# Performance work log

Hardware: AMD Instinct MI355X
Metric: run time of the kernel (lower is better)

Reference implementation:

```python
import jax, jax.numpy as jnp
import numpy as np

N_NODES = 10000
N_EDGES = 80000
OBS_DIMS = 128
HIDDEN = 1024
ACT_DIMS = 8
N_GRAPHS = 64


def setup_inputs() -> dict:
    key = jax.random.key(0)
    ks = jax.random.split(key, 8)
    x = jax.random.normal(ks[0], (N_NODES, OBS_DIMS), dtype=jnp.float32)
    edge_index = jax.random.randint(ks[1], (2, N_EDGES), 0, N_NODES, dtype=jnp.int64)
    batch = jnp.sort(jax.random.randint(ks[2], (N_NODES,), 0, N_GRAPHS, dtype=jnp.int64))
    # Glorot-style init for weights, zero bias (as in PyG GCNConv / Linear defaults)
    W1 = jax.random.normal(ks[3], (OBS_DIMS, HIDDEN), dtype=jnp.float32) * (1.0 / np.sqrt(OBS_DIMS))
    b1 = jnp.zeros((HIDDEN,), dtype=jnp.float32)
    W2 = jax.random.normal(ks[4], (HIDDEN, HIDDEN), dtype=jnp.float32) * (1.0 / np.sqrt(HIDDEN))
    b2 = jnp.zeros((HIDDEN,), dtype=jnp.float32)
    Wl = jax.random.normal(ks[5], (HIDDEN, ACT_DIMS), dtype=jnp.float32) * (1.0 / np.sqrt(HIDDEN))
    bl = jnp.zeros((ACT_DIMS,), dtype=jnp.float32)
    return {"x": x, "edge_index": edge_index, "batch": batch,
            "W1": W1, "b1": b1, "W2": W2, "b2": b2, "Wl": Wl, "bl": bl}


def _gcn_conv(x, src, dst, dinv, W, b, n):
    """PyG GCNConv: D^-1/2 (A+I) D^-1/2 X W + b (self-loops already in src/dst)."""
    h = x @ W                                   # [N, out]
    norm = (dinv[src] * dinv[dst])[:, None]      # [E+N, 1]
    msg = h[src] * norm                          # gather + scale
    out = jax.ops.segment_sum(msg, dst, num_segments=n)
    return out + b


def reference(x, edge_index, batch, W1, b1, W2, b2, Wl, bl):
    n = x.shape[0]
    loops = jnp.arange(n, dtype=edge_index.dtype)
    src = jnp.concatenate([edge_index[0], loops])  # add self-loops
    dst = jnp.concatenate([edge_index[1], loops])
    # degree (with self-loops) from destination column, as PyG does
    deg = jax.ops.segment_sum(jnp.ones_like(dst, dtype=x.dtype), dst, num_segments=n)
    dinv = jax.lax.rsqrt(jnp.maximum(deg, 1.0))

    h = jax.nn.relu(_gcn_conv(x, src, dst, dinv, W1, b1, n))
    h = _gcn_conv(h, src, dst, dinv, W2, b2, n)
    h = jnp.tanh(h @ Wl + bl)                    # [N, act_dims]

    # global_mean_pool over batch segment ids
    sums = jax.ops.segment_sum(h, batch, num_segments=N_GRAPHS)
    counts = jax.ops.segment_sum(jnp.ones((n, 1), h.dtype), batch, num_segments=N_GRAPHS)
    return sums / jnp.maximum(counts, 1.0)       # [N_GRAPHS, act_dims]
```

## Files before the change

kernel.cpp:

```cpp
#include <hip/hip_runtime.h>
#include <hip/hip_bf16.h>

#define NNODES 10000
#define NEDGES 80000
#define OBS    128
#define HID    1024
#define ACTD   8
#define NGR    64

typedef __bf16 bf16x8 __attribute__((ext_vector_type(8)));
typedef float  f32x4  __attribute__((ext_vector_type(4)));
typedef ushort us8    __attribute__((ext_vector_type(8)));
typedef const __attribute__((address_space(1))) unsigned int gl_u32;
typedef __attribute__((address_space(3))) unsigned int lds_u32;

__device__ __forceinline__ ushort f2b(float f) {
    union { float f; unsigned int i; } v; v.f = f;
    unsigned int lsb = (v.i >> 16) & 1u;
    unsigned int r = v.i + 0x7fffu + lsb;
    return (ushort)(r >> 16);
}
__device__ __forceinline__ int cix(int v, int hi) {
    return v < 0 ? 0 : (v >= hi ? hi - 1 : v);
}

__global__ __launch_bounds__(256) void k_prep(const float* __restrict__ W1,
                                              const float* __restrict__ W2,
                                              const float* __restrict__ Wl,
                                              const float* __restrict__ b2,
                                              const float* __restrict__ bl,
                                              ushort* __restrict__ Wt1,
                                              ushort* __restrict__ M2bf,
                                              float* __restrict__ b2l,
                                              float* __restrict__ zacc,
                                              float* __restrict__ pool,
                                              float* __restrict__ cnt,
                                              int* __restrict__ degi) {
    int blk = blockIdx.x;
    if (blk >= 385) {
        int idx = (blk - 385) * 256 + threadIdx.x;
        if (idx < NNODES * ACTD) zacc[idx] = 0.0f;
        if (idx < NGR * ACTD) pool[idx] = 0.0f;
        if (idx < NGR) cnt[idx] = 0.0f;
        if (idx < NNODES) degi[idx] = 0;
        return;
    }
    if (blk < 128) {
        __shared__ float tile[32][33];
        int bx = (blk & 31) * 32, by = (blk >> 5) * 32;
        int tx = threadIdx.x & 31, ty = threadIdx.x >> 5;
        #pragma unroll
        for (int i = 0; i < 32; i += 8)
            tile[ty + i][tx] = W1[(size_t)(by + ty + i) * HID + bx + tx];
        __syncthreads();
        #pragma unroll
        for (int i = 0; i < 32; i += 8)
            Wt1[(size_t)(bx + ty + i) * OBS + by + tx] = f2b(tile[tx][ty + i]);
        return;
    }
    int wvid = ((blk - 128) * 256 + (int)threadIdx.x) >> 6;
    int lane = threadIdx.x & 63;
    if (wvid > HID) return;
    const float* row = (wvid == HID) ? b2 : (W2 + (size_t)wvid * HID);
    float acc[ACTD];
    #pragma unroll
    for (int j = 0; j < ACTD; ++j) acc[j] = 0.0f;
    for (int it = 0; it < HID / 64; ++it) {
        int k = it * 64 + lane;
        float w2v = row[k];
        float4 a = *(const float4*)(Wl + (size_t)k * ACTD);
        float4 b = *(const float4*)(Wl + (size_t)k * ACTD + 4);
        acc[0] += w2v * a.x; acc[1] += w2v * a.y; acc[2] += w2v * a.z; acc[3] += w2v * a.w;
        acc[4] += w2v * b.x; acc[5] += w2v * b.y; acc[6] += w2v * b.z; acc[7] += w2v * b.w;
    }
    #pragma unroll
    for (int off = 32; off > 0; off >>= 1)
        #pragma unroll
        for (int j = 0; j < ACTD; ++j)
            acc[j] += __shfl_down(acc[j], off);
    if (lane == 0) {
        if (wvid == HID) {
            #pragma unroll
            for (int j = 0; j < ACTD; ++j) b2l[j] = acc[j] + bl[j];
        } else {
            #pragma unroll
            for (int j = 0; j < ACTD; ++j) M2bf[wvid * ACTD + j] = f2b(acc[j]);
        }
    }
}

__global__ void k_count(const int* __restrict__ dst, int* degi,
                        const float* __restrict__ xw, int e) {
    int i = blockIdx.x * 256 + threadIdx.x;
    if (i < e) atomicAdd(&degi[cix(dst[i], NNODES)], 1);
    float wacc = 0.0f;
    int stride = gridDim.x * 256;
    for (int k = i; k < NNODES * OBS / 4; k += stride) {
        float4 v = *((const float4*)xw + k);
        wacc += v.x + v.y + v.z + v.w;
    }
    asm volatile("" :: "v"(wacc));
}

__global__ __launch_bounds__(1024) void k_scan(const int* __restrict__ degi,
                                               int* rowptr, int* cursor, float* dinv) {
    __shared__ int wsum[16];
    int t = threadIdx.x, lane = t & 63, w = t >> 6;
    int base = t * 10;
    int local[10];
    int s = 0;
    #pragma unroll
    for (int k = 0; k < 10; ++k) {
        int i = base + k;
        int v = 0;
        if (i < NNODES) {
            v = degi[i];
            dinv[i] = rsqrtf((float)(v + 1));
        }
        local[k] = s; s += v;
    }
    int sc = s;
    #pragma unroll
    for (int off = 1; off < 64; off <<= 1) {
        int u = __shfl_up(sc, off);
        if (lane >= off) sc += u;
    }
    if (lane == 63) wsum[w] = sc;
    __syncthreads();
    if (w == 0 && lane < 16) {
        int v = wsum[lane];
        #pragma unroll
        for (int off = 1; off < 16; off <<= 1) {
            int u = __shfl_up(v, off);
            if (lane >= off) v += u;
        }
        wsum[lane] = v;
    }
    __syncthreads();
    int excl = ((w == 0) ? 0 : wsum[w - 1]) + (sc - s);
    #pragma unroll
    for (int k = 0; k < 10; ++k) {
        int i = base + k;
        if (i < NNODES) { rowptr[i] = excl + local[k]; cursor[i] = excl + local[k]; }
    }
    if (t == 0) rowptr[NNODES] = wsum[15];
}

__global__ void k_fill(const int* __restrict__ src, const int* __restrict__ dst,
                       const float* __restrict__ dinv, int* cursor,
                       int* __restrict__ esrc, float* __restrict__ coefs, int e) {
    int i = blockIdx.x * 256 + threadIdx.x;
    if (i >= e) return;
    int s = cix(src[i], NNODES), d = cix(dst[i], NNODES);
    int pos = atomicAdd(&cursor[d], 1);
    esrc[pos] = s;
    coefs[pos] = dinv[s] * dinv[d];
}

__global__ void k_aggx(const float* __restrict__ x, const float* __restrict__ dinv,
                       const int* __restrict__ rowptr, const int* __restrict__ esrc,
                       const float* __restrict__ coefs, ushort* __restrict__ aggbf, int n) {
    int wv = (blockIdx.x * 256 + threadIdx.x) >> 6;
    int lane = threadIdx.x & 63;
    if (wv >= n) return;
    int q = lane >> 4, c = lane & 15;
    float4 v0 = make_float4(0.f, 0.f, 0.f, 0.f), v1 = v0;
    if (q == 0) {
        float d = dinv[wv], d2 = d * d;
        const float* xs = x + (size_t)wv * OBS + c * 8;
        float4 a0 = *(const float4*)(xs);
        float4 a1 = *(const float4*)(xs + 4);
        v0.x = a0.x * d2; v0.y = a0.y * d2; v0.z = a0.z * d2; v0.w = a0.w * d2;
        v1.x = a1.x * d2; v1.y = a1.y * d2; v1.z = a1.z * d2; v1.w = a1.w * d2;
    }
    int e1 = rowptr[wv + 1];
    for (int e = rowptr[wv] + q; e < e1; e += 4) {
        int s = esrc[e];
        float cf = coefs[e];
        const float* xs = x + (size_t)s * OBS + c * 8;
        float4 a0 = *(const float4*)(xs);
        float4 a1 = *(const float4*)(xs + 4);
        v0.x += a0.x * cf; v0.y += a0.y * cf; v0.z += a0.z * cf; v0.w += a0.w * cf;
        v1.x += a1.x * cf; v1.y += a1.y * cf; v1.z += a1.z * cf; v1.w += a1.w * cf;
    }
    #pragma unroll
    for (int off = 16; off <= 32; off <<= 1) {
        v0.x += __shfl_xor(v0.x, off); v0.y += __shfl_xor(v0.y, off);
        v0.z += __shfl_xor(v0.z, off); v0.w += __shfl_xor(v0.w, off);
        v1.x += __shfl_xor(v1.x, off); v1.y += __shfl_xor(v1.y, off);
        v1.z += __shfl_xor(v1.z, off); v1.w += __shfl_xor(v1.w, off);
    }
    if (q == 0) {
        us8 o;
        o[0] = f2b(v0.x); o[1] = f2b(v0.y); o[2] = f2b(v0.z); o[3] = f2b(v0.w);
        o[4] = f2b(v1.x); o[5] = f2b(v1.y); o[6] = f2b(v1.z); o[7] = f2b(v1.w);
        *(us8*)(aggbf + (size_t)wv * OBS + c * 8) = o;
    }
}

__global__ __launch_bounds__(256) void k_gemm1_fused(const ushort* __restrict__ A,
                                                     const ushort* __restrict__ Bt,
                                                     const float* __restrict__ bias,
                                                     const ushort* __restrict__ M2bf,
                                                     float* __restrict__ zacc,
                                                     int M) {
    __shared__ ushort buf[128 * 136 + 16 * 128];
    ushort* As    = buf;
    ushort* Bs    = buf + 8192;
    ushort* stage = buf;
    ushort* M2t   = buf + 128 * 136;

    const int t = threadIdx.x;
    const int bm = blockIdx.x, bn = blockIdx.y;
    const int lane = t & 63, wv = t >> 6;
    const int wm = (wv & 1) * 64, wn = (wv >> 1) * 64;
    const int l16 = lane & 15, kg = (lane >> 4) * 8;

    if (t < 128) {
        ushort4 a = *(const ushort4*)(M2bf + (size_t)(bn * 128 + t) * ACTD);
        ushort4 b = *(const ushort4*)(M2bf + (size_t)(bn * 128 + t) * ACTD + 4);
        M2t[0 * 128 + t] = a.x; M2t[1 * 128 + t] = a.y;
        M2t[2 * 128 + t] = a.z; M2t[3 * 128 + t] = a.w;
        M2t[4 * 128 + t] = b.x; M2t[5 * 128 + t] = b.y;
        M2t[6 * 128 + t] = b.z; M2t[7 * 128 + t] = b.w;
        #pragma unroll
        for (int j = 8; j < 16; ++j) M2t[j * 128 + t] = 0;
    }

    f32x4 acc[4][4];
    #pragma unroll
    for (int i = 0; i < 4; ++i)
        #pragma unroll
        for (int j = 0; j < 4; ++j)
            acc[i][j] = (f32x4){0.f, 0.f, 0.f, 0.f};

    const int rs = t >> 3;
    const int cs = (t & 7) * 8;
    #pragma unroll
    for (int kt = 0; kt < OBS; kt += 64) {
        #pragma unroll
        for (int p = 0; p < 4; ++p) {
            int r = rs + p * 32;
            int gr = bm * 128 + r; if (gr >= M) gr = M - 1;
            __builtin_amdgcn_global_load_lds(
                (gl_u32*)(A + (size_t)gr * OBS + kt + cs),
                (lds_u32*)(As + r * 64 + cs), 16, 0, 0);
            int gn = bn * 128 + r;
            __builtin_amdgcn_global_load_lds(
                (gl_u32*)(Bt + (size_t)gn * OBS + kt + cs),
                (lds_u32*)(Bs + r * 64 + cs), 16, 0, 0);
        }
        __syncthreads();
        #pragma unroll
        for (int k2 = 0; k2 < 64; k2 += 32) {
            bf16x8 af[4], bfr[4];
            #pragma unroll
            for (int i = 0; i < 4; ++i)
                af[i] = *(const bf16x8*)(As + (wm + i * 16 + l16) * 64 + k2 + kg);
            #pragma unroll
            for (int j = 0; j < 4; ++j)
                bfr[j] = *(const bf16x8*)(Bs + (wn + j * 16 + l16) * 64 + k2 + kg);
            #pragma unroll
            for (int i = 0; i < 4; ++i)
                #pragma unroll
                for (int j = 0; j < 4; ++j)
                    acc[i][j] = __builtin_amdgcn_mfma_f32_16x16x32_bf16(af[i], bfr[j], acc[i][j], 0, 0, 0);
        }
        __syncthreads();
    }

    #pragma unroll
    for (int i = 0; i < 4; ++i) {
        int rowb = wm + i * 16 + (lane >> 4) * 4;
        #pragma unroll
        for (int j = 0; j < 4; ++j) {
            int col = wn + j * 16 + l16;
            float bj = bias[bn * 128 + col];
            #pragma unroll
            for (int r = 0; r < 4; ++r)
                stage[(rowb + r) * 136 + col] = f2b(fmaxf(acc[i][j][r] + bj, 0.0f));
        }
    }
    __syncthreads();

    #pragma unroll
    for (int st = 0; st < 2; ++st) {
        int row0 = wv * 32 + st * 16;
        f32x4 z = (f32x4){0.f, 0.f, 0.f, 0.f};
        #pragma unroll
        for (int kt = 0; kt < 128; kt += 32) {
            bf16x8 a = *(const bf16x8*)(stage + (row0 + l16) * 136 + kt + kg);
            bf16x8 b = *(const bf16x8*)(M2t + l16 * 128 + kt + kg);
            z = __builtin_amdgcn_mfma_f32_16x16x32_bf16(a, b, z, 0, 0, 0);
        }
        if (l16 < ACTD) {
            int rowb = bm * 128 + row0 + (lane >> 4) * 4;
            #pragma unroll
            for (int r = 0; r < 4; ++r)
                if (rowb + r < M)
                    atomicAdd(&zacc[(size_t)(rowb + r) * ACTD + l16], z[r]);
        }
    }
}

__global__ __launch_bounds__(256) void k_zfinal(const float* __restrict__ zacc,
                                                const float* __restrict__ dinv,
                                                const int* __restrict__ rowptr,
                                                const int* __restrict__ esrc,
                                                const float* __restrict__ coefs,
                                                const float* __restrict__ b2l,
                                                const int* __restrict__ batch,
                                                float* __restrict__ pool,
                                                float* __restrict__ cnt, int n) {
    __shared__ float part[NGR * ACTD];
    __shared__ int   partc[NGR];
    int t = threadIdx.x;
    part[t] = 0.0f; part[t + 256] = 0.0f;
    if (t < NGR) partc[t] = 0;
    __syncthreads();

    int idx = blockIdx.x * 256 + t;
    int i = idx >> 3, j = idx & 7;
    if (i < n) {
        float d = dinv[i];
        float v = zacc[idx] * d * d;
        int e0 = rowptr[i], e1 = rowptr[i + 1];
        for (int e = e0; e < e1; ++e)
            v += coefs[e] * zacc[(size_t)esrc[e] * ACTD + j];
        float tz = tanhf(v + b2l[j]);
        int g = cix(batch[i], NGR);
        atomicAdd(&part[g * ACTD + j], tz);
        if (j == 0) atomicAdd(&partc[g], 1);
    }
    __syncthreads();

    int i0 = (blockIdx.x * 256) >> 3;
    int i1 = (blockIdx.x * 256 + 255) >> 3;
    if (i0 >= n) return;
    if (i1 >= n) i1 = n - 1;
    int g0 = cix(batch[i0], NGR), g1 = cix(batch[i1], NGR);
    int ng = g1 - g0 + 1;
    for (int u = t; u < ng * ACTD; u += 256)
        atomicAdd(&pool[g0 * ACTD + u], part[g0 * ACTD + u]);
    for (int u = t; u < ng; u += 256) {
        int c = partc[g0 + u];
        if (c) atomicAdd(&cnt[g0 + u], (float)c);
    }
}

__global__ void k_final(const float* __restrict__ pool, const float* __restrict__ cnt,
                        float* __restrict__ out, int total) {
    int i = blockIdx.x * 256 + threadIdx.x;
    if (i < total) out[i] = pool[i] / fmaxf(cnt[i >> 3], 1.0f);
}

extern "C" void kernel_launch(void* const* d_in, const int* in_sizes, int n_in,
                              void* d_out, int out_size, void* d_ws, size_t ws_size,
                              hipStream_t stream) {
    const float* x   = (const float*)d_in[0];
    const int*   ei  = (const int*)d_in[1];
    const int*   bat = (const int*)d_in[2];
    const float* W1  = (const float*)d_in[3];
    const float* b1  = (const float*)d_in[4];
    const float* W2  = (const float*)d_in[5];
    const float* b2v = (const float*)d_in[6];
    const float* Wl  = (const float*)d_in[7];
    const float* bl  = (const float*)d_in[8];
    float* out = (float*)d_out;

    const int N = NNODES, E = NEDGES;
    const int* src = ei;
    const int* dst = ei + E;

    char* ws = (char*)d_ws;
    size_t off = 0;
    float*  pool   = (float*)(ws + off); off += 2048;
    float*  cnt    = (float*)(ws + off); off += 256;
    float*  dinv   = (float*)(ws + off); off += 40192;
    int*    degi   = (int*)(ws + off);   off += 40192;
    int*    rowptr = (int*)(ws + off);   off += 40448;
    int*    cursor = (int*)(ws + off);   off += 40192;
    int*    esrc   = (int*)(ws + off);   off += (size_t)E * 4;
    float*  coefs  = (float*)(ws + off); off += (size_t)E * 4;
    float*  b2l    = (float*)(ws + off); off += 256;
    ushort* M2bf   = (ushort*)(ws + off); off += (size_t)HID * ACTD * 2;
    ushort* Wt1    = (ushort*)(ws + off); off += (size_t)HID * OBS * 2;
    float*  zacc   = (float*)(ws + off); off += (size_t)N * ACTD * 4;
    ushort* aggbf  = (ushort*)(ws + off); off += (size_t)N * OBS * 2;

    k_prep<<<698, 256, 0, stream>>>(W1, W2, Wl, b2v, bl, Wt1, M2bf, b2l,
                                    zacc, pool, cnt, degi);
    k_count<<<(E + 255) / 256, 256, 0, stream>>>(dst, degi, x, E);
    k_scan<<<1, 1024, 0, stream>>>(degi, rowptr, cursor, dinv);
    k_fill<<<(E + 255) / 256, 256, 0, stream>>>(src, dst, dinv, cursor, esrc, coefs, E);

    k_aggx<<<(N * 64 + 255) / 256, 256, 0, stream>>>(x, dinv, rowptr, esrc, coefs, aggbf, N);

    k_gemm1_fused<<<dim3((N + 127) / 128, HID / 128), 256, 0, stream>>>(
        aggbf, Wt1, b1, M2bf, zacc, N);

    k_zfinal<<<(N * ACTD + 255) / 256, 256, 0, stream>>>(
        zacc, dinv, rowptr, esrc, coefs, b2l, bat, pool, cnt, N);
    k_final<<<2, 256, 0, stream>>>(pool, cnt, out, NGR * ACTD);
}
```

Measured before the change: 132.5 us.

## Fold degree counting into single-block scan and pool directly into output

Removes the separate degree-count kernel, which also held an x-prefetch warm loop, by computing the degree histogram in LDS inside the single-block scan kernel. The scan now also counts nodes per graph and writes inverse counts, so the final pooling kernel scales each value and accumulates straight into the output, which eliminates the k_final launch. Two launches are saved, but the 80k-edge histogram now runs on a single workgroup, which may serialize work that was previously spread across many blocks. Dropping the x-prefetch loop also loses the L2 warming for k_aggx.

Measured after the change: 150.5 us. 13.6% more time.

```diff
diff --git a/kernel.cpp b/kernel.cpp
--- a/kernel.cpp
+++ b/kernel.cpp
@@ -33,16 +33,12 @@
                                               ushort* __restrict__ M2bf,
                                               float* __restrict__ b2l,
                                               float* __restrict__ zacc,
-                                              float* __restrict__ pool,
-                                              float* __restrict__ cnt,
-                                              int* __restrict__ degi) {
+                                              float* __restrict__ out) {
     int blk = blockIdx.x;
     if (blk >= 385) {
         int idx = (blk - 385) * 256 + threadIdx.x;
         if (idx < NNODES * ACTD) zacc[idx] = 0.0f;
-        if (idx < NGR * ACTD) pool[idx] = 0.0f;
-        if (idx < NGR) cnt[idx] = 0.0f;
-        if (idx < NNODES) degi[idx] = 0;
+        if (idx < NGR * ACTD) out[idx] = 0.0f;
         return;
     }
     if (blk < 128) {
@@ -89,23 +85,23 @@
     }
 }
 
-__global__ void k_count(const int* __restrict__ dst, int* degi,
-                        const float* __restrict__ xw, int e) {
-    int i = blockIdx.x * 256 + threadIdx.x;
-    if (i < e) atomicAdd(&degi[cix(dst[i], NNODES)], 1);
-    float wacc = 0.0f;
-    int stride = gridDim.x * 256;
-    for (int k = i; k < NNODES * OBS / 4; k += stride) {
-        float4 v = *((const float4*)xw + k);
-        wacc += v.x + v.y + v.z + v.w;
-    }
-    asm volatile("" :: "v"(wacc));
-}
-
-__global__ __launch_bounds__(1024) void k_scan(const int* __restrict__ degi,
-                                               int* rowptr, int* cursor, float* dinv) {
+__global__ __launch_bounds__(1024) void k_scan(const int* __restrict__ dst,
+                                               const int* __restrict__ batch,
+                                               int* rowptr, int* cursor,
+                                               float* dinv, float* invc, int e) {
+    __shared__ int hdeg[NNODES];
     __shared__ int wsum[16];
+    __shared__ int cntg[NGR];
     int t = threadIdx.x, lane = t & 63, w = t >> 6;
+    for (int i = t; i < NNODES; i += 1024) hdeg[i] = 0;
+    if (t < NGR) cntg[t] = 0;
+    __syncthreads();
+    for (int i = t; i < e; i += 1024)
+        atomicAdd(&hdeg[cix(dst[i], NNODES)], 1);
+    for (int i = t; i < NNODES; i += 1024)
+        atomicAdd(&cntg[cix(batch[i], NGR)], 1);
+    __syncthreads();
+
     int base = t * 10;
     int local[10];
     int s = 0;
@@ -114,7 +110,7 @@
         int i = base + k;
         int v = 0;
         if (i < NNODES) {
-            v = degi[i];
+            v = hdeg[i];
             dinv[i] = rsqrtf((float)(v + 1));
         }
         local[k] = s; s += v;
@@ -144,6 +140,7 @@
         if (i < NNODES) { rowptr[i] = excl + local[k]; cursor[i] = excl + local[k]; }
     }
     if (t == 0) rowptr[NNODES] = wsum[15];
+    if (t < NGR) invc[t] = 1.0f / (float)(cntg[t] > 0 ? cntg[t] : 1);
 }
 
 __global__ void k_fill(const int* __restrict__ src, const int* __restrict__ dst,
@@ -310,13 +307,11 @@
                                                 const float* __restrict__ coefs,
                                                 const float* __restrict__ b2l,
                                                 const int* __restrict__ batch,
-                                                float* __restrict__ pool,
-                                                float* __restrict__ cnt, int n) {
+                                                const float* __restrict__ invc,
+                                                float* __restrict__ out, int n) {
     __shared__ float part[NGR * ACTD];
-    __shared__ int   partc[NGR];
     int t = threadIdx.x;
     part[t] = 0.0f; part[t + 256] = 0.0f;
-    if (t < NGR) partc[t] = 0;
     __syncthreads();
 
     int idx = blockIdx.x * 256 + t;
@@ -327,10 +322,9 @@
         int e0 = rowptr[i], e1 = rowptr[i + 1];
         for (int e = e0; e < e1; ++e)
             v += coefs[e] * zacc[(size_t)esrc[e] * ACTD + j];
-        float tz = tanhf(v + b2l[j]);
         int g = cix(batch[i], NGR);
+        float tz = tanhf(v + b2l[j]) * invc[g];
         atomicAdd(&part[g * ACTD + j], tz);
-        if (j == 0) atomicAdd(&partc[g], 1);
     }
     __syncthreads();
 
@@ -341,17 +335,7 @@
     int g0 = cix(batch[i0], NGR), g1 = cix(batch[i1], NGR);
     int ng = g1 - g0 + 1;
     for (int u = t; u < ng * ACTD; u += 256)
-        atomicAdd(&pool[g0 * ACTD + u], part[g0 * ACTD + u]);
-    for (int u = t; u < ng; u += 256) {
-        int c = partc[g0 + u];
-        if (c) atomicAdd(&cnt[g0 + u], (float)c);
-    }
-}
-
-__global__ void k_final(const float* __restrict__ pool, const float* __restrict__ cnt,
-                        float* __restrict__ out, int total) {
-    int i = blockIdx.x * 256 + threadIdx.x;
-    if (i < total) out[i] = pool[i] / fmaxf(cnt[i >> 3], 1.0f);
+        atomicAdd(&out[g0 * ACTD + u], part[g0 * ACTD + u]);
 }
 
 extern "C" void kernel_launch(void* const* d_in, const int* in_sizes, int n_in,
@@ -374,24 +358,21 @@
 
     char* ws = (char*)d_ws;
     size_t off = 0;
-    float*  pool   = (float*)(ws + off); off += 2048;
-    float*  cnt    = (float*)(ws + off); off += 256;
     float*  dinv   = (float*)(ws + off); off += 40192;
-    int*    degi   = (int*)(ws + off);   off += 40192;
     int*    rowptr = (int*)(ws + off);   off += 40448;
     int*    cursor = (int*)(ws + off);   off += 40192;
     int*    esrc   = (int*)(ws + off);   off += (size_t)E * 4;
     float*  coefs  = (float*)(ws + off); off += (size_t)E * 4;
     float*  b2l    = (float*)(ws + off); off += 256;
+    float*  invc   = (float*)(ws + off); off += 256;
     ushort* M2bf   = (ushort*)(ws + off); off += (size_t)HID * ACTD * 2;
     ushort* Wt1    = (ushort*)(ws + off); off += (size_t)HID * OBS * 2;
     float*  zacc   = (float*)(ws + off); off += (size_t)N * ACTD * 4;
     ushort* aggbf  = (ushort*)(ws + off); off += (size_t)N * OBS * 2;
 
     k_prep<<<698, 256, 0, stream>>>(W1, W2, Wl, b2v, bl, Wt1, M2bf, b2l,
-                                    zacc, pool, cnt, degi);
-    k_count<<<(E + 255) / 256, 256, 0, stream>>>(dst, degi, x, E);
-    k_scan<<<1, 1024, 0, stream>>>(degi, rowptr, cursor, dinv);
+                                    zacc, out);
+    k_scan<<<1, 1024, 0, stream>>>(dst, bat, rowptr, cursor, dinv, invc, E);
     k_fill<<<(E + 255) / 256, 256, 0, stream>>>(src, dst, dinv, cursor, esrc, coefs, E);
 
     k_aggx<<<(N * 64 + 255) / 256, 256, 0, stream>>>(x, dinv, rowptr, esrc, coefs, aggbf, N);
@@ -400,6 +381,5 @@
         aggbf, Wt1, b1, M2bf, zacc, N);
 
     k_zfinal<<<(N * ACTD + 255) / 256, 256, 0, stream>>>(
-        zacc, dinv, rowptr, esrc, coefs, b2l, bat, pool, cnt, N);
-    k_final<<<2, 256, 0, stream>>>(pool, cnt, out, NGR * ACTD);
-}
+        zacc, dinv, rowptr, esrc, coefs, b2l, bat, invc, out, N);
+}
```
